# Optimization experiments

Hardware: AMD Instinct MI355X
Metric: run time of the kernel (lower is better)

Reference implementation:

```python
import jax, jax.numpy as jnp
import numpy as np

D, L, DIM, G = 64, 64, 512, 256      # dialogues, utterances/dialogue, feat dim, graph dim
TOPK_FRAC = 0.2
TAU = 0.07


def setup_inputs() -> dict:
    key = jax.random.key(0)
    ks = jax.random.split(key, 7)
    N = D * L
    t = jax.random.normal(ks[0], (N, DIM), dtype=jnp.float32)
    a = jax.random.normal(ks[1], (N, DIM), dtype=jnp.float32)
    v = jax.random.normal(ks[2], (N, DIM), dtype=jnp.float32)
    W_fc = jax.random.normal(ks[3], (DIM, G), dtype=jnp.float32) / np.sqrt(DIM)
    b_fc = jnp.zeros((G,), dtype=jnp.float32)
    W_h = jax.random.normal(ks[4], (G, G), dtype=jnp.float32) / np.sqrt(G)
    b_h = jnp.zeros((G,), dtype=jnp.float32)
    dia_len = np.full((D,), L, dtype=np.int64)  # uniform dialogue lengths
    return {"t": t, "a": a, "v": v, "W_fc": W_fc, "b_fc": b_fc,
            "W_h": W_h, "b_h": b_h, "dia_len": dia_len}


def _contrastive_loss(x, y, tau=TAU):
    # symmetric InfoNCE with matched-index positives
    xn = x / (jnp.linalg.norm(x, axis=-1, keepdims=True) + 1e-8)
    yn = y / (jnp.linalg.norm(y, axis=-1, keepdims=True) + 1e-8)
    sim = (xn @ yn.T) / tau                     # [N, N]
    pos_xy = jnp.diagonal(jax.nn.log_softmax(sim, axis=1))
    pos_yx = jnp.diagonal(jax.nn.log_softmax(sim, axis=0))
    return -(pos_xy.mean() + pos_yx.mean()) / 2.0


def _forward(t, a, v, W_fc, b_fc, W_h, b_h, dia_len):
    dl = np.asarray(dia_len)
    d, l = dl.shape[0], int(dl[0])              # uniform lengths assumed
    m = 3 * l                                   # nodes (and hyperedges) per dialogue
    k = int(l * TOPK_FRAC)
    dim = t.shape[-1]

    # per-dialogue node features in original order [t_i; a_i; v_i]
    feat = jnp.concatenate([t.reshape(d, l, dim),
                            a.reshape(d, l, dim),
                            v.reshape(d, l, dim)], axis=1)   # [d, m, dim]

    # squared euclidean distances (same ordering as torch.cdist for top-k smallest)
    sq = jnp.sum(feat * feat, axis=-1)                        # [d, m]
    d2 = sq[:, :, None] + sq[:, None, :] - 2.0 * jnp.einsum('dmf,dnf->dmn', feat, feat)
    d2 = jax.lax.stop_gradient(jnp.maximum(d2, 0.0))
    _, idx = jax.lax.top_k(-d2, k)                            # [d, m, k] nearest nodes

    # boolean incidence H[d, e, n] = node n participates in hyperedge e
    # (set-union dedup in the original == boolean OR here)
    node_ids = jnp.arange(m)
    H_nb = (idx[..., None] == node_ids).any(axis=2)           # [d, m, m]
    u = node_ids // 3                                         # central utterance of edge j
    cent = ((node_ids[None, :] == u[:, None]) |
            (node_ids[None, :] == u[:, None] + l) |
            (node_ids[None, :] == u[:, None] + 2 * l))        # [m, m]
    H = (H_nb | cent[None]).astype(feat.dtype)                # [d, m, m]

    # fc projection
    X = feat @ W_fc + b_fc                                    # [d, m, G]

    # hypergraph conv: node -> hyperedge (mean) -> node (mean), then Linear+ReLU
    deg_e = H.sum(axis=2, keepdims=True)                      # [d, m, 1]
    E = jnp.einsum('den,dng->deg', H, X) / deg_e              # edge features
    deg_v = H.sum(axis=1)[..., None]                          # [d, m, 1]
    Y = jnp.einsum('den,deg->dng', H, E) / deg_v              # node features
    out = jax.nn.relu(Y @ W_h + b_h)                          # [d, m, G]

    # reverse_features: regroup by modality across dialogues
    tn = out[:, :l].reshape(d * l, -1)
    an = out[:, l:2 * l].reshape(d * l, -1)
    vn = out[:, 2 * l:].reshape(d * l, -1)
    out_cat = jnp.concatenate([tn, an, vn], axis=1)           # [N, 3G]

    loss = (_contrastive_loss(tn, an) + _contrastive_loss(tn, vn)
            + _contrastive_loss(an, vn)) / 3.0
    return out_cat, loss


def reference(t, a, v, W_fc, b_fc, W_h, b_h, dia_len):
    return _forward(t, a, v, W_fc, b_fc, W_h, b_h, dia_len)
```

## Files before the change

kernel.cpp:

```cpp
#include <hip/hip_runtime.h>
#include <math.h>

#define NDIAL 64
#define M3    192
#define DIMF  512
#define GDIM  256
#define NROW  4096
#define TOPK  12
#define INV_TAU (1.0f/0.07f)

typedef __attribute__((ext_vector_type(8))) short bf16x8;
typedef __attribute__((ext_vector_type(4))) float f32x4;
typedef __attribute__((ext_vector_type(8))) ushort us8;
typedef _Float16 f16x8 __attribute__((ext_vector_type(8)));
typedef _Float16 f16x4v __attribute__((ext_vector_type(4)));
typedef __attribute__((address_space(3))) ushort lds_us;
typedef const __attribute__((address_space(1))) ushort gm_us;

__device__ __forceinline__ ushort f2bf(float f) {
    unsigned u = __float_as_uint(f);
    unsigned r = (u + 0x7fff + ((u >> 16) & 1)) >> 16;
    return (ushort)r;
}

template<int KD, int NW>
__device__ __forceinline__ void hgemm_bt(const _Float16* __restrict__ A, int lda,
                                         const _Float16* __restrict__ B, int ldb,
                                         f32x4 acc[4][4]) {
    __shared__ __align__(16) _Float16 As[64 * 40];
    __shared__ __align__(16) _Float16 Bs[NW * 64 * 40];
    const int tid = threadIdx.x;
    const int lane = tid & 63, w = tid >> 6;
    const int qd = lane >> 4, l15 = lane & 15;

#pragma unroll
    for (int fm = 0; fm < 4; fm++)
#pragma unroll
        for (int fn = 0; fn < 4; fn++)
            acc[fm][fn] = (f32x4){0.f, 0.f, 0.f, 0.f};

    for (int k0 = 0; k0 < KD; k0 += 32) {
        for (int f = tid; f < 256; f += NW * 64) {
            int row = f >> 2, c8 = f & 3;
            *(float4*)&As[row * 40 + c8 * 8] =
                *(const float4*)&A[(size_t)row * lda + k0 + c8 * 8];
        }
#pragma unroll
        for (int i = 0; i < 4; i++) {
            int f = tid + i * NW * 64;
            int row = f >> 2, c8 = f & 3;
            *(float4*)&Bs[row * 40 + c8 * 8] =
                *(const float4*)&B[(size_t)row * ldb + k0 + c8 * 8];
        }
        __syncthreads();
        f16x8 af[4], bfr[4];
#pragma unroll
        for (int fm = 0; fm < 4; fm++)
            af[fm] = *(const f16x8*)&As[(fm * 16 + l15) * 40 + qd * 8];
#pragma unroll
        for (int fn = 0; fn < 4; fn++)
            bfr[fn] = *(const f16x8*)&Bs[(w * 64 + fn * 16 + l15) * 40 + qd * 8];
#pragma unroll
        for (int fm = 0; fm < 4; fm++)
#pragma unroll
            for (int fn = 0; fn < 4; fn++)
                acc[fm][fn] = __builtin_amdgcn_mfma_f32_16x16x32_f16(
                    af[fm], bfr[fn], acc[fm][fn], 0, 0, 0);
        __syncthreads();
    }
}

__device__ __forceinline__ const float* node_ptr(const float* t, const float* a,
                                                 const float* v, int d, int j) {
    int mod = j >> 6, i = j & 63;
    const float* base = (mod == 0) ? t : (mod == 1) ? a : v;
    return base + (size_t)(d * 64 + i) * DIMF;
}

__global__ void kprep(const float* __restrict__ t, const float* __restrict__ a,
                      const float* __restrict__ v, const float* __restrict__ Wfc,
                      const float* __restrict__ Wh, _Float16* __restrict__ feath,
                      _Float16* __restrict__ featl, _Float16* __restrict__ featT,
                      _Float16* __restrict__ Wfch, _Float16* __restrict__ WhT,
                      float* __restrict__ sq, float* __restrict__ rs,
                      float* __restrict__ cs, float* __restrict__ degV,
                      _Float16* __restrict__ HbT) {
    int b = blockIdx.x, tid = threadIdx.x;
    if (b < 6144) {
        int e = (b * 256 + tid) * 4;
        int d = e / (M3 * DIMF);
        int rem = e % (M3 * DIMF);
        int n = rem / DIMF, kk = rem % DIMF;
        int mod = n >> 6, i = n & 63;
        const float* src = ((mod == 0) ? t : (mod == 1) ? a : v)
                           + (size_t)(d * 64 + i) * DIMF + kk;
        float4 x = *(const float4*)src;
        f16x4v h = {(_Float16)x.x, (_Float16)x.y, (_Float16)x.z, (_Float16)x.w};
        f16x4v l = {(_Float16)(x.x - (float)h.x), (_Float16)(x.y - (float)h.y),
                    (_Float16)(x.z - (float)h.z), (_Float16)(x.w - (float)h.w)};
        *(f16x4v*)&feath[e] = h;
        *(f16x4v*)&featl[e] = l;
    } else if (b < 6272) {
        int e = ((b - 6144) * 256 + tid) * 4;
        float4 x = *(const float4*)&Wfc[e];
        f16x4v o = {(_Float16)x.x, (_Float16)x.y, (_Float16)x.z, (_Float16)x.w};
        *(f16x4v*)&Wfch[e] = o;
    } else if (b < 6336) {
        int e = ((b - 6272) * 256 + tid) * 4;
        int go = e >> 8, g = e & 255;
        f16x4v o = {(_Float16)Wh[(size_t)(g + 0) * GDIM + go],
                    (_Float16)Wh[(size_t)(g + 1) * GDIM + go],
                    (_Float16)Wh[(size_t)(g + 2) * GDIM + go],
                    (_Float16)Wh[(size_t)(g + 3) * GDIM + go]};
        *(f16x4v*)&WhT[(size_t)go * GDIM + g] = o;
    } else if (b < 9408) {
        int lane = tid & 63, wv = tid >> 6;
        int n = (b - 6336) * 4 + wv;
        int d = n / M3, j = n % M3;
        const float4* s4 = (const float4*)node_ptr(t, a, v, d, j);
        float s = 0.f;
#pragma unroll
        for (int q = 0; q < 2; q++) {
            float4 x = s4[lane + q * 64];
            s += x.x * x.x + x.y * x.y + x.z * x.z + x.w * x.w;
        }
        for (int o = 32; o; o >>= 1) s += __shfl_down(s, o);
        if (lane == 0) sq[n] = s;
    } else if (b < 9456) {
        int i = (b - 9408) * 256 + tid;
        rs[i] = 0.f; cs[i] = 0.f; degV[i] = 0.f;
    } else if (b < 11760) {
        int i = (b - 9456) * 256 + tid;
        ulonglong2 z = {0ull, 0ull};
        *(ulonglong2*)&HbT[(size_t)i * 8] = z;
    } else {
        __shared__ _Float16 tl[64 * 72];
        int idx = b - 11760;
        int d = idx / 24, rem = idx % 24;
        int jb = rem / 8, fb = rem % 8;
        const float* src = ((jb == 0) ? t : (jb == 1) ? a : v)
                           + (size_t)(d * 64) * DIMF + fb * 64;
#pragma unroll
        for (int it = 0; it < 4; it++) {
            int jj = (tid >> 4) + it * 16, ff = (tid & 15) * 4;
            float4 x = *(const float4*)&src[(size_t)jj * DIMF + ff];
            tl[jj * 72 + ff + 0] = (_Float16)x.x;
            tl[jj * 72 + ff + 1] = (_Float16)x.y;
            tl[jj * 72 + ff + 2] = (_Float16)x.z;
            tl[jj * 72 + ff + 3] = (_Float16)x.w;
        }
        __syncthreads();
        _Float16* dst = featT + (size_t)d * DIMF * M3 + (size_t)(fb * 64) * M3 + jb * 64;
#pragma unroll
        for (int it = 0; it < 4; it++) {
            int fr = (tid >> 4) + it * 16, jc = (tid & 15) * 4;
            f16x4v o = {tl[(jc + 0) * 72 + fr], tl[(jc + 1) * 72 + fr],
                        tl[(jc + 2) * 72 + fr], tl[(jc + 3) * 72 + fr]};
            *(f16x4v*)&dst[(size_t)fr * M3 + jc] = o;
        }
    }
}

__global__ void kW(const _Float16* __restrict__ WhT, const _Float16* __restrict__ Wfch,
                   const float* __restrict__ bfc, const float* __restrict__ bh,
                   const float* __restrict__ Wh, _Float16* __restrict__ W2t,
                   float* __restrict__ b2) {
    if (blockIdx.x == 8) {
        int go = threadIdx.x;
        float s = bh[go];
        for (int g = 0; g < GDIM; g++) s += bfc[g] * Wh[(size_t)g * GDIM + go];
        b2[go] = s;
        return;
    }
    int rb = blockIdx.x >> 1, cb = blockIdx.x & 1;
    f32x4 acc[4][4];
    hgemm_bt<GDIM, 4>(WhT + (size_t)rb * 64 * GDIM, GDIM,
                      Wfch + (size_t)cb * 256 * GDIM, GDIM, acc);
    int lane = threadIdx.x & 63, w = threadIdx.x >> 6;
    int qd = lane >> 4, l15 = lane & 15;
#pragma unroll
    for (int fm = 0; fm < 4; fm++)
#pragma unroll
        for (int rg = 0; rg < 4; rg++) {
            int go = rb * 64 + fm * 16 + qd * 4 + rg;
#pragma unroll
            for (int fn = 0; fn < 4; fn++) {
                int f = cb * 256 + w * 64 + fn * 16 + l15;
                W2t[(size_t)go * DIMF + f] = (_Float16)acc[fm][fn][rg];
            }
        }
}

__global__ __launch_bounds__(192) void k1_d2(const _Float16* __restrict__ feath,
                                             const _Float16* __restrict__ featl,
                                             const float* __restrict__ sq,
                                             float* __restrict__ d2) {
    __shared__ __align__(16) _Float16 Ah[64 * 40], Al[64 * 40];
    __shared__ __align__(16) _Float16 Bh[M3 * 40], Bl[M3 * 40];
    int rb = blockIdx.x, d = blockIdx.y;
    const _Float16* ah = feath + ((size_t)d * M3 + rb * 64) * DIMF;
    const _Float16* al = featl + ((size_t)d * M3 + rb * 64) * DIMF;
    const _Float16* bh = feath + (size_t)d * M3 * DIMF;
    const _Float16* bl = featl + (size_t)d * M3 * DIMF;
    const int tid = threadIdx.x;
    const int lane = tid & 63, w = tid >> 6;
    const int qd = lane >> 4, l15 = lane & 15;

    f32x4 acc[4][4] = {};
    for (int k0 = 0; k0 < DIMF; k0 += 32) {
        for (int f = tid; f < 256; f += 192) {
            int row = f >> 2, c8 = f & 3;
            *(float4*)&Ah[row * 40 + c8 * 8] =
                *(const float4*)&ah[(size_t)row * DIMF + k0 + c8 * 8];
            *(float4*)&Al[row * 40 + c8 * 8] =
                *(const float4*)&al[(size_t)row * DIMF + k0 + c8 * 8];
        }
#pragma unroll
        for (int i = 0; i < 4; i++) {
            int f = tid + i * 192;
            int row = f >> 2, c8 = f & 3;
            *(float4*)&Bh[row * 40 + c8 * 8] =
                *(const float4*)&bh[(size_t)row * DIMF + k0 + c8 * 8];
            *(float4*)&Bl[row * 40 + c8 * 8] =
                *(const float4*)&bl[(size_t)row * DIMF + k0 + c8 * 8];
        }
        __syncthreads();
        f16x8 afh[4], afl[4], bfh[4], bfl[4];
#pragma unroll
        for (int fm = 0; fm < 4; fm++) {
            afh[fm] = *(const f16x8*)&Ah[(fm * 16 + l15) * 40 + qd * 8];
            afl[fm] = *(const f16x8*)&Al[(fm * 16 + l15) * 40 + qd * 8];
        }
#pragma unroll
        for (int fn = 0; fn < 4; fn++) {
            bfh[fn] = *(const f16x8*)&Bh[(w * 64 + fn * 16 + l15) * 40 + qd * 8];
            bfl[fn] = *(const f16x8*)&Bl[(w * 64 + fn * 16 + l15) * 40 + qd * 8];
        }
#pragma unroll
        for (int fm = 0; fm < 4; fm++)
#pragma unroll
            for (int fn = 0; fn < 4; fn++) {
                acc[fm][fn] = __builtin_amdgcn_mfma_f32_16x16x32_f16(
                    afh[fm], bfh[fn], acc[fm][fn], 0, 0, 0);
                acc[fm][fn] = __builtin_amdgcn_mfma_f32_16x16x32_f16(
                    afh[fm], bfl[fn], acc[fm][fn], 0, 0, 0);
                acc[fm][fn] = __builtin_amdgcn_mfma_f32_16x16x32_f16(
                    afl[fm], bfh[fn], acc[fm][fn], 0, 0, 0);
            }
        __syncthreads();
    }
    const float* sqd = sq + d * M3;
    float* outp = d2 + (size_t)d * M3 * M3;
#pragma unroll
    for (int fm = 0; fm < 4; fm++)
#pragma unroll
        for (int rg = 0; rg < 4; rg++) {
            int il = rb * 64 + fm * 16 + qd * 4 + rg;
            float si = sqd[il];
#pragma unroll
            for (int fn = 0; fn < 4; fn++) {
                int jl = w * 64 + fn * 16 + l15;
                outp[(size_t)il * M3 + jl] =
                    fmaxf(si + sqd[jl] - 2.f * acc[fm][fn][rg], 0.f);
            }
        }
}

__global__ void k2_topk(const float* __restrict__ d2, _Float16* __restrict__ HbT,
                        _Float16* __restrict__ HbTd, float* __restrict__ degV) {
    int lane = threadIdx.x & 63, wv = threadIdx.x >> 6;
    int r = blockIdx.x * 4 + wv;
    int d = r / M3, e = r % M3;
    const float* row = d2 + (size_t)r * M3;
    float w0 = row[lane], w1 = row[lane + 64], w2 = row[lane + 128];
    bool s0 = false, s1 = false, s2 = false;
#pragma unroll
    for (int it = 0; it < TOPK; it++) {
        float bv = w0; int bi = lane;
        if (w1 < bv) { bv = w1; bi = lane + 64; }
        if (w2 < bv) { bv = w2; bi = lane + 128; }
#pragma unroll
        for (int o = 1; o < 64; o <<= 1) {
            float ov = __shfl_xor(bv, o);
            int   oi = __shfl_xor(bi, o);
            if (ov < bv || (ov == bv && oi < bi)) { bv = ov; bi = oi; }
        }
        if (bi == lane)            { s0 = true; w0 = 3.4e38f; }
        else if (bi == lane + 64)  { s1 = true; w1 = 3.4e38f; }
        else if (bi == lane + 128) { s2 = true; w2 = 3.4e38f; }
    }
    int u = e / 3;
    if (lane == u) { s0 = true; s1 = true; s2 = true; }
    float cnt = (s0 ? 1.f : 0.f) + (s1 ? 1.f : 0.f) + (s2 ? 1.f : 0.f);
#pragma unroll
    for (int o = 1; o < 64; o <<= 1) cnt += __shfl_xor(cnt, o);
    _Float16 rde = (_Float16)(1.f / cnt);
    float* dv = degV + d * M3;
    _Float16* HT  = HbT  + (size_t)d * M3 * M3;
    _Float16* HTd = HbTd + (size_t)d * M3 * M3;
    if (s0) { atomicAdd(&dv[lane], 1.f);
              HT[(size_t)lane * M3 + e] = (_Float16)1.f;
              HTd[(size_t)lane * M3 + e] = rde; }
    if (s1) { atomicAdd(&dv[lane + 64], 1.f);
              HT[(size_t)(lane + 64) * M3 + e] = (_Float16)1.f;
              HTd[(size_t)(lane + 64) * M3 + e] = rde; }
    if (s2) { atomicAdd(&dv[lane + 128], 1.f);
              HT[(size_t)(lane + 128) * M3 + e] = (_Float16)1.f;
              HTd[(size_t)(lane + 128) * M3 + e] = rde; }
}

__global__ __launch_bounds__(192) void kM(const _Float16* __restrict__ HbT,
                                          const _Float16* __restrict__ HbTd,
                                          _Float16* __restrict__ S) {
    int rb = blockIdx.x, d = blockIdx.y;
    f32x4 acc[4][4];
    hgemm_bt<M3, 3>(HbT + (size_t)d * M3 * M3 + (size_t)rb * 64 * M3, M3,
                    HbTd + (size_t)d * M3 * M3, M3, acc);
    int lane = threadIdx.x & 63, w = threadIdx.x >> 6;
    int qd = lane >> 4, l15 = lane & 15;
    _Float16* out = S + (size_t)d * M3 * M3;
#pragma unroll
    for (int fm = 0; fm < 4; fm++)
#pragma unroll
        for (int rg = 0; rg < 4; rg++) {
            int i = rb * 64 + fm * 16 + qd * 4 + rg;
#pragma unroll
            for (int fn = 0; fn < 4; fn++) {
                int j = w * 64 + fn * 16 + l15;
                out[(size_t)i * M3 + j] = (_Float16)acc[fm][fn][rg];
            }
        }
}

__global__ void kZ(const _Float16* __restrict__ S, const _Float16* __restrict__ featT,
                   const float* __restrict__ degV, _Float16* __restrict__ Z) {
    int rb = blockIdx.x % 3, cb = blockIdx.x / 3, d = blockIdx.y;
    f32x4 acc[4][4];
    hgemm_bt<M3, 4>(S + (size_t)d * M3 * M3 + (size_t)rb * 64 * M3, M3,
                    featT + (size_t)d * DIMF * M3 + (size_t)cb * 256 * M3, M3, acc);
    int lane = threadIdx.x & 63, w = threadIdx.x >> 6;
    int qd = lane >> 4, l15 = lane & 15;
#pragma unroll
    for (int fm = 0; fm < 4; fm++)
#pragma unroll
        for (int rg = 0; rg < 4; rg++) {
            int node = rb * 64 + fm * 16 + qd * 4 + rg;
            float idv = 1.f / degV[d * M3 + node];
            _Float16* zr = Z + ((size_t)d * M3 + node) * DIMF + cb * 256;
#pragma unroll
            for (int fn = 0; fn < 4; fn++) {
                int f = w * 64 + fn * 16 + l15;
                zr[f] = (_Float16)(acc[fm][fn][rg] * idv);
            }
        }
}

__global__ __launch_bounds__(256) void kO(const _Float16* __restrict__ Z,
                                          const _Float16* __restrict__ W2t,
                                          const float* __restrict__ b2,
                                          float* __restrict__ outp,
                                          ushort* __restrict__ xnb) {
    __shared__ float tile[64 * 256];
    __shared__ float ssq[64];
    int b = blockIdx.x, tid = threadIdx.x;
    if (tid < 64) ssq[tid] = 0.f;
    f32x4 acc[4][4];
    hgemm_bt<DIMF, 4>(Z + (size_t)b * 64 * DIMF, DIMF, W2t, DIMF, acc);
    int lane = tid & 63, w = tid >> 6;
    int qd = lane >> 4, l15 = lane & 15;
    int d = b / 3, mod = b % 3;
    float bb[4];
#pragma unroll
    for (int fn = 0; fn < 4; fn++)
        bb[fn] = b2[w * 64 + fn * 16 + l15];
#pragma unroll
    for (int fm = 0; fm < 4; fm++)
#pragma unroll
        for (int rg = 0; rg < 4; rg++) {
            int i = fm * 16 + qd * 4 + rg;
            float* orow = outp + (size_t)(d * 64 + i) * 768 + mod * GDIM;
            float s2 = 0.f;
#pragma unroll
            for (int fn = 0; fn < 4; fn++) {
                int go = w * 64 + fn * 16 + l15;
                float vv = fmaxf(acc[fm][fn][rg] + bb[fn], 0.f);
                orow[go] = vv;
                tile[i * 256 + go] = vv;
                s2 += vv * vv;
            }
            s2 += __shfl_xor(s2, 1);
            s2 += __shfl_xor(s2, 2);
            s2 += __shfl_xor(s2, 4);
            s2 += __shfl_xor(s2, 8);
            if (l15 == 0) atomicAdd(&ssq[i], s2);
        }
    __syncthreads();
    if (tid < 64) ssq[tid] = 1.f / (sqrtf(ssq[tid]) + 1e-8f);
    __syncthreads();
#pragma unroll
    for (int it = 0; it < 8; it++) {
        int f = tid + it * 256;
        int row = f >> 5, c = f & 31;
        float4 xa = *(const float4*)&tile[row * 256 + c * 8];
        float4 xb = *(const float4*)&tile[row * 256 + c * 8 + 4];
        float iv = ssq[row];
        us8 o = {f2bf(xa.x * iv), f2bf(xa.y * iv), f2bf(xa.z * iv), f2bf(xa.w * iv),
                 f2bf(xb.x * iv), f2bf(xb.y * iv), f2bf(xb.z * iv), f2bf(xb.w * iv)};
        int rx = d * 64 + row;
        int slot = (c & 24) | ((c & 7) ^ (row & 7));
        *(us8*)&xnb[((size_t)mod * NROW + rx) * GDIM + slot * 8] = o;
    }
}

#define TILE2 256
__global__ __launch_bounds__(512, 2) void k9_mfma(const ushort* __restrict__ xnb,
                                                  float* __restrict__ rs,
                                                  float* __restrict__ cs,
                                                  float* __restrict__ diag) {
    int cj = blockIdx.x, ci = blockIdx.y, p = blockIdx.z;
    int px = (p == 2) ? 1 : 0;
    int py = (p == 0) ? 1 : 2;
    const ushort* A = xnb + ((size_t)px * NROW + ci * TILE2) * GDIM;
    const ushort* B = xnb + ((size_t)py * NROW + cj * TILE2) * GDIM;

    __shared__ __align__(16) ushort As[TILE2 * 64];
    __shared__ __align__(16) ushort Bs[TILE2 * 64];

    const int tid = threadIdx.x;
    const int lane = tid & 63, w = tid >> 6;
    const int wrow = w >> 2, wcol = w & 3;
    const int qd = lane >> 4, l15 = lane & 15;
    const int lrow = lane >> 3, lslot = lane & 7;

    f32x4 acc[8][4] = {};

    for (int kh = 0; kh < 4; kh++) {
#pragma unroll
        for (int j = 0; j < 4; j++) {
            int rr = w * 32 + j * 8 + lrow;
            __builtin_amdgcn_global_load_lds(
                (gm_us*)(A + (size_t)rr * GDIM + kh * 64 + lslot * 8),
                (lds_us*)&As[(w * 32 + j * 8) * 64], 16, 0, 0);
            __builtin_amdgcn_global_load_lds(
                (gm_us*)(B + (size_t)rr * GDIM + kh * 64 + lslot * 8),
                (lds_us*)&Bs[(w * 32 + j * 8) * 64], 16, 0, 0);
        }
        __syncthreads();
#pragma unroll
        for (int kk = 0; kk < 2; kk++) {
            bf16x8 af[8], bfv[4];
#pragma unroll
            for (int fm = 0; fm < 8; fm++) {
                int ar = wrow * 128 + fm * 16 + l15;
                af[fm] = *(const bf16x8*)&As[ar * 64 + ((kk * 4 + qd) ^ (ar & 7)) * 8];
            }
#pragma unroll
            for (int fn = 0; fn < 4; fn++) {
                int br = wcol * 64 + fn * 16 + l15;
                bfv[fn] = *(const bf16x8*)&Bs[br * 64 + ((kk * 4 + qd) ^ (br & 7)) * 8];
            }
#pragma unroll
            for (int fm = 0; fm < 8; fm++)
#pragma unroll
                for (int fn = 0; fn < 4; fn++)
                    acc[fm][fn] = __builtin_amdgcn_mfma_f32_16x16x32_bf16(
                        af[fm], bfv[fn], acc[fm][fn], 0, 0, 0);
        }
        __syncthreads();
    }

    float rloc[8][4] = {};
    float cloc[4] = {};
#pragma unroll
    for (int fm = 0; fm < 8; fm++)
#pragma unroll
        for (int fn = 0; fn < 4; fn++)
#pragma unroll
            for (int rg = 0; rg < 4; rg++) {
                float s = acc[fm][fn][rg] * INV_TAU;
                float e = __expf(s);
                rloc[fm][rg] += e;
                cloc[fn] += e;
                int grow = ci * TILE2 + wrow * 128 + fm * 16 + qd * 4 + rg;
                int gcol = cj * TILE2 + wcol * 64 + fn * 16 + l15;
                if (grow == gcol) diag[p * NROW + grow] = s;
            }
#pragma unroll
    for (int fm = 0; fm < 8; fm++)
#pragma unroll
        for (int rg = 0; rg < 4; rg++) {
            float s = rloc[fm][rg];
            s += __shfl_xor(s, 1);
            s += __shfl_xor(s, 2);
            s += __shfl_xor(s, 4);
            s += __shfl_xor(s, 8);
            if (l15 == 0)
                atomicAdd(&rs[p * NROW + ci * TILE2 + wrow * 128 + fm * 16 + qd * 4 + rg], s);
        }
#pragma unroll
    for (int fn = 0; fn < 4; fn++) {
        float s = cloc[fn];
        s += __shfl_xor(s, 16);
        s += __shfl_xor(s, 32);
        if (qd == 0)
            atomicAdd(&cs[p * NROW + cj * TILE2 + wcol * 64 + fn * 16 + l15], s);
    }
}

__global__ void k10_loss(const float* __restrict__ diag, const float* __restrict__ rs,
                         const float* __restrict__ cs, float* __restrict__ outp) {
    float acc = 0.f;
    for (int i = threadIdx.x; i < 3 * NROW; i += 256)
        acc += 2.f * diag[i] - logf(rs[i]) - logf(cs[i]);
    int lane = threadIdx.x & 63, wv = threadIdx.x >> 6;
    for (int o = 32; o; o >>= 1) acc += __shfl_down(acc, o);
    __shared__ float red[4];
    if (lane == 0) red[wv] = acc;
    __syncthreads();
    if (threadIdx.x == 0) {
        float tot = red[0] + red[1] + red[2] + red[3];
        outp[(size_t)NROW * 768] = -tot / (NROW * 6.0f);
    }
}

extern "C" void kernel_launch(void* const* d_in, const int* in_sizes, int n_in,
                              void* d_out, int out_size, void* d_ws, size_t ws_size,
                              hipStream_t stream) {
    const float* t   = (const float*)d_in[0];
    const float* a   = (const float*)d_in[1];
    const float* v   = (const float*)d_in[2];
    const float* Wfc = (const float*)d_in[3];
    const float* bfc = (const float*)d_in[4];
    const float* Wh  = (const float*)d_in[5];
    const float* bh  = (const float*)d_in[6];
    float* outp = (float*)d_out;
    float* ws = (float*)d_ws;

    float* sq    = ws;
    float* d2F   = sq + 12288;
    float* HbTF  = d2F + 2359296;
    float* HbTdF = HbTF + 1179648;
    float* degV  = HbTdF + 1179648;
    float* feathF= degV + 12288;
    float* featlF= feathF + 3145728;
    float* featTF= featlF + 3145728;
    float* WfchF = featTF + 3145728;
    float* WhTF  = WfchF + 65536;
    float* W2tF  = WhTF + 32768;
    float* b2    = W2tF + 65536;
    float* rs    = b2 + 256;
    float* cs    = rs + 12288;
    float* diag  = cs + 12288;

    _Float16* HbT   = (_Float16*)HbTF;
    _Float16* HbTd  = (_Float16*)HbTdF;
    _Float16* feath = (_Float16*)feathF;
    _Float16* featl = (_Float16*)featlF;
    _Float16* featT = (_Float16*)featTF;
    _Float16* Wfch  = (_Float16*)WfchF;
    _Float16* WhT   = (_Float16*)WhTF;
    _Float16* W2t   = (_Float16*)W2tF;
    _Float16* S     = (_Float16*)featlF;
    _Float16* Z     = (_Float16*)feathF;
    ushort*   xnb   = (ushort*)d2F;

    kprep  <<<13296, 256, 0, stream>>>(t, a, v, Wfc, Wh, feath, featl, featT,
                                       Wfch, WhT, sq, rs, cs, degV, HbT);
    kW     <<<9, 256, 0, stream>>>(WhT, Wfch, bfc, bh, Wh, W2t, b2);
    k1_d2  <<<dim3(3, 64), 192, 0, stream>>>(feath, featl, sq, d2F);
    k2_topk<<<3072, 256, 0, stream>>>(d2F, HbT, HbTd, degV);
    kM     <<<dim3(3, 64), 192, 0, stream>>>(HbT, HbTd, S);
    kZ     <<<dim3(6, 64), 256, 0, stream>>>(S, featT, degV, Z);
    kO     <<<192, 256, 0, stream>>>(Z, W2t, b2, outp, xnb);
    k9_mfma<<<dim3(16, 16, 3), 512, 0, stream>>>(xnb, rs, cs, diag);
    k10_loss<<<1, 256, 0, stream>>>(diag, rs, cs, outp);
}
```

Baseline: 290.3 us.

## Fuse weight precompute into prep, top-k into distance kernel, S into Z GEMM

Folds the W2 = Wh^T·Wfc precompute and the bias fold into kprep as scalar FP32 loops, which removes the separate kW launch and the fp16 weight conversion. The top-k selection now runs inside the distance kernel on an LDS copy of the distances, so the d2 matrix no longer goes through global memory. The H·Hd product S stays in LDS and feeds the Z GEMM in the same kernel. The similarity GEMM also loads 128-wide K chunks with an adjusted swizzle. Together these cut three launches and several global round trips. In exchange the W2 compute is a slow scalar loop, the top-k work is spread over only 192 blocks, and the fused kernels use more LDS, which can lower occupancy.

```diff
diff --git a/kernel.cpp b/kernel.cpp
--- a/kernel.cpp
+++ b/kernel.cpp
@@ -79,12 +79,14 @@
 
 __global__ void kprep(const float* __restrict__ t, const float* __restrict__ a,
                       const float* __restrict__ v, const float* __restrict__ Wfc,
-                      const float* __restrict__ Wh, _Float16* __restrict__ feath,
+                      const float* __restrict__ bfc, const float* __restrict__ Wh,
+                      const float* __restrict__ bh, _Float16* __restrict__ feath,
                       _Float16* __restrict__ featl, _Float16* __restrict__ featT,
-                      _Float16* __restrict__ Wfch, _Float16* __restrict__ WhT,
+                      _Float16* __restrict__ W2t, float* __restrict__ b2,
                       float* __restrict__ sq, float* __restrict__ rs,
                       float* __restrict__ cs, float* __restrict__ degV,
                       _Float16* __restrict__ HbT) {
+    __shared__ _Float16 tl[64 * 72];
     int b = blockIdx.x, tid = threadIdx.x;
     if (b < 6144) {
         int e = (b * 256 + tid) * 4;
@@ -100,22 +102,9 @@
                     (_Float16)(x.z - (float)h.z), (_Float16)(x.w - (float)h.w)};
         *(f16x4v*)&feath[e] = h;
         *(f16x4v*)&featl[e] = l;
-    } else if (b < 6272) {
-        int e = ((b - 6144) * 256 + tid) * 4;
-        float4 x = *(const float4*)&Wfc[e];
-        f16x4v o = {(_Float16)x.x, (_Float16)x.y, (_Float16)x.z, (_Float16)x.w};
-        *(f16x4v*)&Wfch[e] = o;
-    } else if (b < 6336) {
-        int e = ((b - 6272) * 256 + tid) * 4;
-        int go = e >> 8, g = e & 255;
-        f16x4v o = {(_Float16)Wh[(size_t)(g + 0) * GDIM + go],
-                    (_Float16)Wh[(size_t)(g + 1) * GDIM + go],
-                    (_Float16)Wh[(size_t)(g + 2) * GDIM + go],
-                    (_Float16)Wh[(size_t)(g + 3) * GDIM + go]};
-        *(f16x4v*)&WhT[(size_t)go * GDIM + g] = o;
-    } else if (b < 9408) {
+    } else if (b < 9216) {
         int lane = tid & 63, wv = tid >> 6;
-        int n = (b - 6336) * 4 + wv;
+        int n = (b - 6144) * 4 + wv;
         int d = n / M3, j = n % M3;
         const float4* s4 = (const float4*)node_ptr(t, a, v, d, j);
         float s = 0.f;
@@ -126,16 +115,15 @@
         }
         for (int o = 32; o; o >>= 1) s += __shfl_down(s, o);
         if (lane == 0) sq[n] = s;
-    } else if (b < 9456) {
-        int i = (b - 9408) * 256 + tid;
+    } else if (b < 9264) {
+        int i = (b - 9216) * 256 + tid;
         rs[i] = 0.f; cs[i] = 0.f; degV[i] = 0.f;
-    } else if (b < 11760) {
-        int i = (b - 9456) * 256 + tid;
+    } else if (b < 11568) {
+        int i = (b - 9264) * 256 + tid;
         ulonglong2 z = {0ull, 0ull};
         *(ulonglong2*)&HbT[(size_t)i * 8] = z;
-    } else {
-        __shared__ _Float16 tl[64 * 72];
-        int idx = b - 11760;
+    } else if (b < 13104) {
+        int idx = b - 11568;
         int d = idx / 24, rem = idx % 24;
         int jb = rem / 8, fb = rem % 8;
         const float* src = ((jb == 0) ? t : (jb == 1) ? a : v)
@@ -158,45 +146,36 @@
                         tl[(jc + 2) * 72 + fr], tl[(jc + 3) * 72 + fr]};
             *(f16x4v*)&dst[(size_t)fr * M3 + jc] = o;
         }
-    }
-}
-
-__global__ void kW(const _Float16* __restrict__ WhT, const _Float16* __restrict__ Wfch,
-                   const float* __restrict__ bfc, const float* __restrict__ bh,
-                   const float* __restrict__ Wh, _Float16* __restrict__ W2t,
-                   float* __restrict__ b2) {
-    if (blockIdx.x == 8) {
-        int go = threadIdx.x;
+    } else if (b < 13232) {
+        int idx = b - 13104;
+        int go = idx * 2 + (tid >> 7);
+        int f0 = (tid & 127) * 4;
+        float s[4] = {0.f, 0.f, 0.f, 0.f};
+        for (int g = 0; g < GDIM; g++) {
+            float wh = Wh[(size_t)g * GDIM + go];
+#pragma unroll
+            for (int i = 0; i < 4; i++)
+                s[i] += Wfc[(size_t)(f0 + i) * GDIM + g] * wh;
+        }
+        f16x4v o = {(_Float16)s[0], (_Float16)s[1], (_Float16)s[2], (_Float16)s[3]};
+        *(f16x4v*)&W2t[(size_t)go * DIMF + f0] = o;
+    } else {
+        int go = tid;
         float s = bh[go];
         for (int g = 0; g < GDIM; g++) s += bfc[g] * Wh[(size_t)g * GDIM + go];
         b2[go] = s;
-        return;
-    }
-    int rb = blockIdx.x >> 1, cb = blockIdx.x & 1;
-    f32x4 acc[4][4];
-    hgemm_bt<GDIM, 4>(WhT + (size_t)rb * 64 * GDIM, GDIM,
-                      Wfch + (size_t)cb * 256 * GDIM, GDIM, acc);
-    int lane = threadIdx.x & 63, w = threadIdx.x >> 6;
-    int qd = lane >> 4, l15 = lane & 15;
-#pragma unroll
-    for (int fm = 0; fm < 4; fm++)
-#pragma unroll
-        for (int rg = 0; rg < 4; rg++) {
-            int go = rb * 64 + fm * 16 + qd * 4 + rg;
-#pragma unroll
-            for (int fn = 0; fn < 4; fn++) {
-                int f = cb * 256 + w * 64 + fn * 16 + l15;
-                W2t[(size_t)go * DIMF + f] = (_Float16)acc[fm][fn][rg];
-            }
-        }
-}
-
-__global__ __launch_bounds__(192) void k1_d2(const _Float16* __restrict__ feath,
-                                             const _Float16* __restrict__ featl,
-                                             const float* __restrict__ sq,
-                                             float* __restrict__ d2) {
+    }
+}
+
+__global__ __launch_bounds__(192) void k1_topk(const _Float16* __restrict__ feath,
+                                               const _Float16* __restrict__ featl,
+                                               const float* __restrict__ sq,
+                                               _Float16* __restrict__ HbT,
+                                               _Float16* __restrict__ HbTd,
+                                               float* __restrict__ degV) {
     __shared__ __align__(16) _Float16 Ah[64 * 40], Al[64 * 40];
     __shared__ __align__(16) _Float16 Bh[M3 * 40], Bl[M3 * 40];
+    __shared__ float d2s[64 * 200];
     int rb = blockIdx.x, d = blockIdx.y;
     const _Float16* ah = feath + ((size_t)d * M3 + rb * 64) * DIMF;
     const _Float16* al = featl + ((size_t)d * M3 + rb * 64) * DIMF;
@@ -250,109 +229,139 @@
         __syncthreads();
     }
     const float* sqd = sq + d * M3;
-    float* outp = d2 + (size_t)d * M3 * M3;
 #pragma unroll
     for (int fm = 0; fm < 4; fm++)
 #pragma unroll
         for (int rg = 0; rg < 4; rg++) {
-            int il = rb * 64 + fm * 16 + qd * 4 + rg;
-            float si = sqd[il];
+            int il = fm * 16 + qd * 4 + rg;
+            float si = sqd[rb * 64 + il];
 #pragma unroll
             for (int fn = 0; fn < 4; fn++) {
                 int jl = w * 64 + fn * 16 + l15;
-                outp[(size_t)il * M3 + jl] =
+                d2s[il * 200 + jl] =
                     fmaxf(si + sqd[jl] - 2.f * acc[fm][fn][rg], 0.f);
             }
         }
-}
-
-__global__ void k2_topk(const float* __restrict__ d2, _Float16* __restrict__ HbT,
-                        _Float16* __restrict__ HbTd, float* __restrict__ degV) {
-    int lane = threadIdx.x & 63, wv = threadIdx.x >> 6;
-    int r = blockIdx.x * 4 + wv;
-    int d = r / M3, e = r % M3;
-    const float* row = d2 + (size_t)r * M3;
-    float w0 = row[lane], w1 = row[lane + 64], w2 = row[lane + 128];
-    bool s0 = false, s1 = false, s2 = false;
-#pragma unroll
-    for (int it = 0; it < TOPK; it++) {
-        float bv = w0; int bi = lane;
-        if (w1 < bv) { bv = w1; bi = lane + 64; }
-        if (w2 < bv) { bv = w2; bi = lane + 128; }
-#pragma unroll
-        for (int o = 1; o < 64; o <<= 1) {
-            float ov = __shfl_xor(bv, o);
-            int   oi = __shfl_xor(bi, o);
-            if (ov < bv || (ov == bv && oi < bi)) { bv = ov; bi = oi; }
-        }
-        if (bi == lane)            { s0 = true; w0 = 3.4e38f; }
-        else if (bi == lane + 64)  { s1 = true; w1 = 3.4e38f; }
-        else if (bi == lane + 128) { s2 = true; w2 = 3.4e38f; }
-    }
-    int u = e / 3;
-    if (lane == u) { s0 = true; s1 = true; s2 = true; }
-    float cnt = (s0 ? 1.f : 0.f) + (s1 ? 1.f : 0.f) + (s2 ? 1.f : 0.f);
-#pragma unroll
-    for (int o = 1; o < 64; o <<= 1) cnt += __shfl_xor(cnt, o);
-    _Float16 rde = (_Float16)(1.f / cnt);
+    __syncthreads();
+
     float* dv = degV + d * M3;
     _Float16* HT  = HbT  + (size_t)d * M3 * M3;
     _Float16* HTd = HbTd + (size_t)d * M3 * M3;
-    if (s0) { atomicAdd(&dv[lane], 1.f);
-              HT[(size_t)lane * M3 + e] = (_Float16)1.f;
-              HTd[(size_t)lane * M3 + e] = rde; }
-    if (s1) { atomicAdd(&dv[lane + 64], 1.f);
-              HT[(size_t)(lane + 64) * M3 + e] = (_Float16)1.f;
-              HTd[(size_t)(lane + 64) * M3 + e] = rde; }
-    if (s2) { atomicAdd(&dv[lane + 128], 1.f);
-              HT[(size_t)(lane + 128) * M3 + e] = (_Float16)1.f;
-              HTd[(size_t)(lane + 128) * M3 + e] = rde; }
-}
-
-__global__ __launch_bounds__(192) void kM(const _Float16* __restrict__ HbT,
-                                          const _Float16* __restrict__ HbTd,
-                                          _Float16* __restrict__ S) {
+    for (int rl = w; rl < 64; rl += 3) {
+        int e = rb * 64 + rl;
+        float w0 = d2s[rl * 200 + lane];
+        float w1 = d2s[rl * 200 + lane + 64];
+        float w2 = d2s[rl * 200 + lane + 128];
+        bool s0 = false, s1 = false, s2 = false;
+#pragma unroll
+        for (int it = 0; it < TOPK; it++) {
+            float bv = w0; int bi = lane;
+            if (w1 < bv) { bv = w1; bi = lane + 64; }
+            if (w2 < bv) { bv = w2; bi = lane + 128; }
+#pragma unroll
+            for (int o = 1; o < 64; o <<= 1) {
+                float ov = __shfl_xor(bv, o);
+                int   oi = __shfl_xor(bi, o);
+                if (ov < bv || (ov == bv && oi < bi)) { bv = ov; bi = oi; }
+            }
+            if (bi == lane)            { s0 = true; w0 = 3.4e38f; }
+            else if (bi == lane + 64)  { s1 = true; w1 = 3.4e38f; }
+            else if (bi == lane + 128) { s2 = true; w2 = 3.4e38f; }
+        }
+        int u = e / 3;
+        if (lane == u) { s0 = true; s1 = true; s2 = true; }
+        float cnt = (s0 ? 1.f : 0.f) + (s1 ? 1.f : 0.f) + (s2 ? 1.f : 0.f);
+#pragma unroll
+        for (int o = 1; o < 64; o <<= 1) cnt += __shfl_xor(cnt, o);
+        _Float16 rde = (_Float16)(1.f / cnt);
+        if (s0) { atomicAdd(&dv[lane], 1.f);
+                  HT[(size_t)lane * M3 + e] = (_Float16)1.f;
+                  HTd[(size_t)lane * M3 + e] = rde; }
+        if (s1) { atomicAdd(&dv[lane + 64], 1.f);
+                  HT[(size_t)(lane + 64) * M3 + e] = (_Float16)1.f;
+                  HTd[(size_t)(lane + 64) * M3 + e] = rde; }
+        if (s2) { atomicAdd(&dv[lane + 128], 1.f);
+                  HT[(size_t)(lane + 128) * M3 + e] = (_Float16)1.f;
+                  HTd[(size_t)(lane + 128) * M3 + e] = rde; }
+    }
+}
+
+__global__ __launch_bounds__(192) void kSZ(const _Float16* __restrict__ HbT,
+                                           const _Float16* __restrict__ HbTd,
+                                           const _Float16* __restrict__ featT,
+                                           const float* __restrict__ degV,
+                                           _Float16* __restrict__ Z) {
+    __shared__ __align__(16) _Float16 Ss[64 * 200];
+    __shared__ __align__(16) _Float16 Bs2[M3 * 40];
     int rb = blockIdx.x, d = blockIdx.y;
+    const int tid = threadIdx.x;
+    const int lane = tid & 63, w = tid >> 6;
+    const int qd = lane >> 4, l15 = lane & 15;
+
     f32x4 acc[4][4];
     hgemm_bt<M3, 3>(HbT + (size_t)d * M3 * M3 + (size_t)rb * 64 * M3, M3,
                     HbTd + (size_t)d * M3 * M3, M3, acc);
-    int lane = threadIdx.x & 63, w = threadIdx.x >> 6;
-    int qd = lane >> 4, l15 = lane & 15;
-    _Float16* out = S + (size_t)d * M3 * M3;
 #pragma unroll
     for (int fm = 0; fm < 4; fm++)
 #pragma unroll
         for (int rg = 0; rg < 4; rg++) {
-            int i = rb * 64 + fm * 16 + qd * 4 + rg;
-#pragma unroll
-            for (int fn = 0; fn < 4; fn++) {
-                int j = w * 64 + fn * 16 + l15;
-                out[(size_t)i * M3 + j] = (_Float16)acc[fm][fn][rg];
-            }
-        }
-}
-
-__global__ void kZ(const _Float16* __restrict__ S, const _Float16* __restrict__ featT,
-                   const float* __restrict__ degV, _Float16* __restrict__ Z) {
-    int rb = blockIdx.x % 3, cb = blockIdx.x / 3, d = blockIdx.y;
-    f32x4 acc[4][4];
-    hgemm_bt<M3, 4>(S + (size_t)d * M3 * M3 + (size_t)rb * 64 * M3, M3,
-                    featT + (size_t)d * DIMF * M3 + (size_t)cb * 256 * M3, M3, acc);
-    int lane = threadIdx.x & 63, w = threadIdx.x >> 6;
-    int qd = lane >> 4, l15 = lane & 15;
+            int i = fm * 16 + qd * 4 + rg;
+#pragma unroll
+            for (int fn = 0; fn < 4; fn++)
+                Ss[i * 200 + w * 64 + fn * 16 + l15] = (_Float16)acc[fm][fn][rg];
+        }
+    __syncthreads();
+
+    float idv[4][4];
 #pragma unroll
     for (int fm = 0; fm < 4; fm++)
 #pragma unroll
-        for (int rg = 0; rg < 4; rg++) {
-            int node = rb * 64 + fm * 16 + qd * 4 + rg;
-            float idv = 1.f / degV[d * M3 + node];
-            _Float16* zr = Z + ((size_t)d * M3 + node) * DIMF + cb * 256;
-#pragma unroll
-            for (int fn = 0; fn < 4; fn++) {
-                int f = w * 64 + fn * 16 + l15;
-                zr[f] = (_Float16)(acc[fm][fn][rg] * idv);
-            }
-        }
+        for (int rg = 0; rg < 4; rg++)
+            idv[fm][rg] = 1.f / degV[d * M3 + rb * 64 + fm * 16 + qd * 4 + rg];
+
+    const _Float16* fT = featT + (size_t)d * DIMF * M3;
+    for (int pb = 0; pb < 3; pb++) {
+        int ncols = (pb == 2) ? 128 : 192;
+        bool active = (w * 64 < ncols);
+        f32x4 a2[4][4] = {};
+        for (int k0 = 0; k0 < M3; k0 += 32) {
+            for (int f = tid; f < ncols * 4; f += 192) {
+                int row = f >> 2, c8 = f & 3;
+                *(float4*)&Bs2[row * 40 + c8 * 8] =
+                    *(const float4*)&fT[(size_t)(pb * 192 + row) * M3 + k0 + c8 * 8];
+            }
+            __syncthreads();
+            if (active) {
+                f16x8 af[4], bf[4];
+#pragma unroll
+                for (int fm = 0; fm < 4; fm++)
+                    af[fm] = *(const f16x8*)&Ss[(fm * 16 + l15) * 200 + k0 + qd * 8];
+#pragma unroll
+                for (int fn = 0; fn < 4; fn++)
+                    bf[fn] = *(const f16x8*)&Bs2[(w * 64 + fn * 16 + l15) * 40 + qd * 8];
+#pragma unroll
+                for (int fm = 0; fm < 4; fm++)
+#pragma unroll
+                    for (int fn = 0; fn < 4; fn++)
+                        a2[fm][fn] = __builtin_amdgcn_mfma_f32_16x16x32_f16(
+                            af[fm], bf[fn], a2[fm][fn], 0, 0, 0);
+            }
+            __syncthreads();
+        }
+        if (active) {
+#pragma unroll
+            for (int fm = 0; fm < 4; fm++)
+#pragma unroll
+                for (int rg = 0; rg < 4; rg++) {
+                    int node = rb * 64 + fm * 16 + qd * 4 + rg;
+                    _Float16* zr = Z + ((size_t)d * M3 + node) * DIMF + pb * 192;
+#pragma unroll
+                    for (int fn = 0; fn < 4; fn++)
+                        zr[w * 64 + fn * 16 + l15] =
+                            (_Float16)(a2[fm][fn][rg] * idv[fm][rg]);
+                }
+        }
+    }
 }
 
 __global__ __launch_bounds__(256) void kO(const _Float16* __restrict__ Z,
@@ -423,41 +432,44 @@
     const ushort* A = xnb + ((size_t)px * NROW + ci * TILE2) * GDIM;
     const ushort* B = xnb + ((size_t)py * NROW + cj * TILE2) * GDIM;
 
-    __shared__ __align__(16) ushort As[TILE2 * 64];
-    __shared__ __align__(16) ushort Bs[TILE2 * 64];
+    __shared__ __align__(16) ushort As[TILE2 * 128];
+    __shared__ __align__(16) ushort Bs[TILE2 * 128];
 
     const int tid = threadIdx.x;
     const int lane = tid & 63, w = tid >> 6;
     const int wrow = w >> 2, wcol = w & 3;
     const int qd = lane >> 4, l15 = lane & 15;
-    const int lrow = lane >> 3, lslot = lane & 7;
+    const int lrow = lane >> 4, lslot = lane & 15;
 
     f32x4 acc[8][4] = {};
 
-    for (int kh = 0; kh < 4; kh++) {
-#pragma unroll
-        for (int j = 0; j < 4; j++) {
-            int rr = w * 32 + j * 8 + lrow;
+    for (int kh = 0; kh < 2; kh++) {
+#pragma unroll
+        for (int j = 0; j < 8; j++) {
+            int rr = w * 32 + j * 4 + lrow;
             __builtin_amdgcn_global_load_lds(
-                (gm_us*)(A + (size_t)rr * GDIM + kh * 64 + lslot * 8),
-                (lds_us*)&As[(w * 32 + j * 8) * 64], 16, 0, 0);
+                (gm_us*)(A + (size_t)rr * GDIM + kh * 128 + lslot * 8),
+                (lds_us*)&As[(w * 32 + j * 4) * 128], 16, 0, 0);
             __builtin_amdgcn_global_load_lds(
-                (gm_us*)(B + (size_t)rr * GDIM + kh * 64 + lslot * 8),
-                (lds_us*)&Bs[(w * 32 + j * 8) * 64], 16, 0, 0);
-        }
-        __syncthreads();
-#pragma unroll
-        for (int kk = 0; kk < 2; kk++) {
+                (gm_us*)(B + (size_t)rr * GDIM + kh * 128 + lslot * 8),
+                (lds_us*)&Bs[(w * 32 + j * 4) * 128], 16, 0, 0);
+        }
+        __syncthreads();
+#pragma unroll
+        for (int kk = 0; kk < 4; kk++) {
+            int lc = kk * 4 + qd;
             bf16x8 af[8], bfv[4];
 #pragma unroll
             for (int fm = 0; fm < 8; fm++) {
                 int ar = wrow * 128 + fm * 16 + l15;
-                af[fm] = *(const bf16x8*)&As[ar * 64 + ((kk * 4 + qd) ^ (ar & 7)) * 8];
+                int sl = (lc & 8) | ((lc & 7) ^ (ar & 7));
+                af[fm] = *(const bf16x8*)&As[ar * 128 + sl * 8];
             }
 #pragma unroll
             for (int fn = 0; fn < 4; fn++) {
                 int br = wcol * 64 + fn * 16 + l15;
-                bfv[fn] = *(const bf16x8*)&Bs[br * 64 + ((kk * 4 + qd) ^ (br & 7)) * 8];
+                int sl = (lc & 8) | ((lc & 7) ^ (br & 7));
+                bfv[fn] = *(const bf16x8*)&Bs[br * 128 + sl * 8];
             }
 #pragma unroll
             for (int fm = 0; fm < 8; fm++)
@@ -536,41 +548,33 @@
     float* outp = (float*)d_out;
     float* ws = (float*)d_ws;
 
-    float* sq    = ws;
-    float* d2F   = sq + 12288;
-    float* HbTF  = d2F + 2359296;
-    float* HbTdF = HbTF + 1179648;
-    float* degV  = HbTdF + 1179648;
-    float* feathF= degV + 12288;
-    float* featlF= feathF + 3145728;
-    float* featTF= featlF + 3145728;
-    float* WfchF = featTF + 3145728;
-    float* WhTF  = WfchF + 65536;
-    float* W2tF  = WhTF + 32768;
-    float* b2    = W2tF + 65536;
-    float* rs    = b2 + 256;
-    float* cs    = rs + 12288;
-    float* diag  = cs + 12288;
+    float* sq     = ws;
+    float* xnbF   = sq + 12288;
+    float* HbTF   = xnbF + 1572864;
+    float* HbTdF  = HbTF + 1179648;
+    float* degV   = HbTdF + 1179648;
+    float* feathF = degV + 12288;
+    float* featlF = feathF + 3145728;
+    float* featTF = featlF + 3145728;
+    float* W2tF   = featTF + 3145728;
+    float* b2     = W2tF + 65536;
+    float* rs     = b2 + 256;
+    float* cs     = rs + 12288;
+    float* diag   = cs + 12288;
 
     _Float16* HbT   = (_Float16*)HbTF;
     _Float16* HbTd  = (_Float16*)HbTdF;
     _Float16* feath = (_Float16*)feathF;
     _Float16* featl = (_Float16*)featlF;
     _Float16* featT = (_Float16*)featTF;
-    _Float16* Wfch  = (_Float16*)WfchF;
-    _Float16* WhT   = (_Float16*)WhTF;
     _Float16* W2t   = (_Float16*)W2tF;
-    _Float16* S     = (_Float16*)featlF;
     _Float16* Z     = (_Float16*)feathF;
-    ushort*   xnb   = (ushort*)d2F;
-
-    kprep  <<<13296, 256, 0, stream>>>(t, a, v, Wfc, Wh, feath, featl, featT,
-                                       Wfch, WhT, sq, rs, cs, degV, HbT);
-    kW     <<<9, 256, 0, stream>>>(WhT, Wfch, bfc, bh, Wh, W2t, b2);
-    k1_d2  <<<dim3(3, 64), 192, 0, stream>>>(feath, featl, sq, d2F);
-    k2_topk<<<3072, 256, 0, stream>>>(d2F, HbT, HbTd, degV);
-    kM     <<<dim3(3, 64), 192, 0, stream>>>(HbT, HbTd, S);
-    kZ     <<<dim3(6, 64), 256, 0, stream>>>(S, featT, degV, Z);
+    ushort*   xnb   = (ushort*)xnbF;
+
+    kprep  <<<13233, 256, 0, stream>>>(t, a, v, Wfc, bfc, Wh, bh, feath, featl,
+                                       featT, W2t, b2, sq, rs, cs, degV, HbT);
+    k1_topk<<<dim3(3, 64), 192, 0, stream>>>(feath, featl, sq, HbT, HbTd, degV);
+    kSZ    <<<dim3(3, 64), 192, 0, stream>>>(HbT, HbTd, featT, degV, Z);
     kO     <<<192, 256, 0, stream>>>(Z, W2t, b2, outp, xnb);
     k9_mfma<<<dim3(16, 16, 3), 512, 0, stream>>>(xnb, rs, cs, diag);
     k10_loss<<<1, 256, 0, stream>>>(diag, rs, cs, outp);
```

After: 472.1 us. 1.63x slower.
